# Kernel tuning notes

Hardware: AMD Instinct MI355X
Metric: run time of the kernel (lower is better)

Reference implementation:

```python
import jax, jax.numpy as jnp
import numpy as np

MASK_INFTY_APPROX = 1e30
B, L, D = 2, 2048, 1024
H = 16
HD = D // H  # 64
NCODE = 512


def setup_inputs() -> dict:
    key = jax.random.key(0)
    ks = jax.random.split(key, 6)
    s = 1.0 / np.sqrt(D)
    x = jax.random.normal(ks[0], (B, L, D), dtype=jnp.float32)
    Wq = jax.random.normal(ks[1], (D, D), dtype=jnp.float32) * s
    Wk = jax.random.normal(ks[2], (D, D), dtype=jnp.float32) * s
    Wv = jax.random.normal(ks[3], (D, D), dtype=jnp.float32) * s
    Wo = jax.random.normal(ks[4], (D, D), dtype=jnp.float32) * s
    codebook = jax.random.normal(ks[5], (H, NCODE, HD), dtype=jnp.float32)
    return {"x": x, "Wq": Wq, "Wk": Wk, "Wv": Wv, "Wo": Wo, "codebook": codebook}


def _vq(k, codebook):
    # k: [B,H,L,hd], codebook: [H,C,hd]
    dot = jnp.einsum('bhld,hcd->bhlc', k, codebook)
    k2 = jnp.sum(k * k, axis=-1, keepdims=True)            # [B,H,L,1]
    c2 = jnp.sum(codebook * codebook, axis=-1)             # [H,C]
    d2 = k2 - 2.0 * dot + c2[None, :, None, :]             # [B,H,L,C]
    shortcodes = jnp.argmin(d2, axis=-1)                   # [B,H,L]
    h_idx = jnp.arange(H)[None, :, None]
    c_sel = codebook[h_idx, shortcodes]                    # [B,H,L,hd]
    # straight-through quantization
    k_hat = k + jax.lax.stop_gradient(c_sel - k)
    l_commit = jnp.mean(jnp.sum((k - jax.lax.stop_gradient(c_sel)) ** 2, axis=-1))
    l_codebook = jnp.mean(jnp.sum((jax.lax.stop_gradient(k) - c_sel) ** 2, axis=-1))
    return k_hat, shortcodes, l_commit, l_codebook


def reference(x, Wq, Wk, Wv, Wo, codebook):
    q = jnp.einsum('bld,de->ble', x, Wq.T).reshape(B, L, H, HD).transpose(0, 2, 1, 3)
    k = jnp.einsum('bld,de->ble', x, Wk.T).reshape(B, L, H, HD).transpose(0, 2, 1, 3)
    v = jnp.einsum('bld,de->ble', x, Wv.T).reshape(B, L, H, HD).transpose(0, 2, 1, 3)
    k_hat, shortcodes, l_commit, l_codebook = _vq(k, codebook)
    scale = HD ** (-0.5)
    logits = jnp.einsum('bhld,bhtd->bhlt', q, k_hat) * scale  # [B,H,L,L]
    causal_mask = jnp.tril(jnp.ones((L, L), dtype=bool))
    logits = jnp.where(causal_mask[None, None], logits, -MASK_INFTY_APPROX)
    w = jax.nn.softmax(logits, axis=-1)
    attn = jnp.einsum('bhlt,bhtd->bhld', w, v)
    attn = attn.transpose(0, 2, 1, 3).reshape(B, L, D)
    out = jnp.einsum('bld,de->ble', attn, Wo.T)
    return out, l_commit, l_codebook, shortcodes
```

## Files before the change

kernel.cpp:

```cpp
#include <hip/hip_runtime.h>
#include <stdint.h>

#define BB 2
#define HH 16
#define LL 2048
#define DD 1024
#define HDD 64
#define NC 512

typedef __bf16 bf16x8 __attribute__((ext_vector_type(8)));
typedef float f32x4 __attribute__((ext_vector_type(4)));
typedef unsigned short u16x8 __attribute__((ext_vector_type(8)));

__device__ __forceinline__ unsigned short f2bf(float f) {
  union { float f; unsigned u; } v; v.f = f;
  unsigned u = v.u;
  u += 0x7fffu + ((u >> 16) & 1u);
  return (unsigned short)(u >> 16);
}
__device__ __forceinline__ float bf2f(unsigned short h) {
  union { unsigned u; float f; } v; v.u = ((unsigned)h) << 16;
  return v.f;
}

__device__ __forceinline__ void load_lds16(const unsigned short* g, unsigned short* l) {
  __builtin_amdgcn_global_load_lds((const __attribute__((address_space(1))) void*)g,
                                   (__attribute__((address_space(3))) void*)l, 16, 0, 0);
}

__global__ void cast_all(const float* __restrict__ x, const float* __restrict__ wq,
                         const float* __restrict__ wk, const float* __restrict__ wv,
                         const float* __restrict__ wo, const float* __restrict__ cb,
                         unsigned short* __restrict__ xb, unsigned short* __restrict__ xl,
                         unsigned short* __restrict__ wb, unsigned short* __restrict__ wkl,
                         unsigned short* __restrict__ wob, unsigned short* __restrict__ cbb,
                         unsigned short* __restrict__ cbl, float* __restrict__ lsum) {
  long i = (long)blockIdx.x * blockDim.x + threadIdx.x;
  if (i == 0) lsum[0] = 0.f;
  const long NX = 4194304, NW = 1048576, NCB = 524288;
  const long TOT = NX + 4 * NW + NCB;
  for (long t = i; t < TOT; t += (long)gridDim.x * blockDim.x) {
    if (t < NX) {
      float v = x[t];
      unsigned short hi = f2bf(v);
      xb[t] = hi;
      xl[t] = f2bf(v - bf2f(hi));
    } else if (t < NX + NW) {
      wb[t - NX] = f2bf(wq[t - NX]);
    } else if (t < NX + 2 * NW) {
      long idx = t - NX - NW;
      float v = wk[idx];
      unsigned short hi = f2bf(v);
      wb[NW + idx] = hi;
      wkl[idx] = f2bf(v - bf2f(hi));
    } else if (t < NX + 3 * NW) {
      wb[t - NX] = f2bf(wv[t - NX - 2 * NW]);
    } else if (t < NX + 4 * NW) {
      wob[t - NX - 3 * NW] = f2bf(wo[t - NX - 3 * NW]);
    } else {
      long idx = t - NX - 4 * NW;
      float v = cb[idx];
      unsigned short hi = f2bf(v);
      cbb[idx] = hi;
      cbl[idx] = f2bf(v - bf2f(hi));
    }
  }
}

__global__ void c2_kernel(const float* __restrict__ cb, float* __restrict__ c2) {
  int i = blockIdx.x * blockDim.x + threadIdx.x;
  if (i >= HH * NC) return;
  const float* r = cb + (long)i * HDD;
  double s = 0.0;
  for (int j = 0; j < HDD; j++) s += (double)r[j] * (double)r[j];
  c2[i] = (float)s;
}

__global__ __launch_bounds__(256) void gemm_qv(
    const unsigned short* __restrict__ xb, const unsigned short* __restrict__ wb,
    unsigned short* __restrict__ qb, unsigned short* __restrict__ vt) {
  __shared__ __align__(16) unsigned short As[128 * 32];
  __shared__ __align__(16) unsigned short Bs[128 * 32];
  int tid = threadIdx.x;
  int wave = tid >> 6, lane = tid & 63;
  int quad = lane >> 4, col = lane & 15;
  int m0 = blockIdx.y * 128;
  int n0 = blockIdx.x * 128 + (blockIdx.x >= 8 ? 1024 : 0);
  f32x4 acc[4][4] = {};
  int row_in = (wave << 4) + (lane >> 2);
  int seg = lane & 3;
  const unsigned short* gA0 = xb + (long)(m0 + row_in) * DD + seg * 8;
  const unsigned short* gA1 = xb + (long)(m0 + 64 + row_in) * DD + seg * 8;
  const unsigned short* gB0 = wb + (long)(n0 + row_in) * DD + seg * 8;
  const unsigned short* gB1 = wb + (long)(n0 + 64 + row_in) * DD + seg * 8;
  unsigned short* lA0 = As + wave * 512;
  unsigned short* lA1 = As + 2048 + wave * 512;
  unsigned short* lB0 = Bs + wave * 512;
  unsigned short* lB1 = Bs + 2048 + wave * 512;
  int wm = wave & 1, wn = wave >> 1;
  const unsigned short* pa = As + (wm * 64 + col) * 32 + quad * 8;
  const unsigned short* pb = Bs + (wn * 64 + col) * 32 + quad * 8;
  for (int kk = 0; kk < DD; kk += 32) {
    __syncthreads();
    load_lds16(gA0 + kk, lA0);
    load_lds16(gA1 + kk, lA1);
    load_lds16(gB0 + kk, lB0);
    load_lds16(gB1 + kk, lB1);
    __syncthreads();
    bf16x8 af[4], bfr[4];
    for (int t = 0; t < 4; t++) af[t]  = *(const bf16x8*)(pa + t * 512);
    for (int t = 0; t < 4; t++) bfr[t] = *(const bf16x8*)(pb + t * 512);
    for (int mt = 0; mt < 4; mt++)
      for (int nt = 0; nt < 4; nt++)
        acc[mt][nt] = __builtin_amdgcn_mfma_f32_16x16x32_bf16(af[mt], bfr[nt], acc[mt][nt], 0, 0, 0);
  }
  for (int mt = 0; mt < 4; mt++)
    for (int nt = 0; nt < 4; nt++) {
      int mbase = m0 + wm * 64 + mt * 16 + quad * 4;
      int n = n0 + wn * 64 + nt * 16 + col;
      int which = n >> 10, e = n & 1023;
      int h = e >> 6, hd = e & 63;
      for (int r = 0; r < 4; r++) {
        int m = mbase + r;
        int b = m >> 11, l = m & 2047;
        unsigned short val = f2bf(acc[mt][nt][r]);
        long bh = (long)(b * HH + h);
        if (which == 0)      qb[(bh * LL + l) * HDD + hd] = val;
        else                 vt[(bh * HDD + hd) * LL + l] = val;
      }
    }
}

__global__ __launch_bounds__(256) void kgemm_split(
    const unsigned short* __restrict__ xb, const unsigned short* __restrict__ xl,
    const unsigned short* __restrict__ wb, const unsigned short* __restrict__ wkl,
    float* __restrict__ kf) {
  __shared__ __align__(16) unsigned short Ah[128 * 32];
  __shared__ __align__(16) unsigned short Al[128 * 32];
  __shared__ __align__(16) unsigned short Bh[64 * 32];
  __shared__ __align__(16) unsigned short Bl[64 * 32];
  int tid = threadIdx.x;
  int wave = tid >> 6, lane = tid & 63;
  int quad = lane >> 4, col = lane & 15;
  int n0 = blockIdx.x * 64;
  int m0 = blockIdx.y * 128;
  f32x4 acc[4][2] = {};
  int row_in = (wave << 4) + (lane >> 2);
  int seg = lane & 3;
  const unsigned short* gAh0 = xb + (long)(m0 + row_in) * DD + seg * 8;
  const unsigned short* gAh1 = xb + (long)(m0 + 64 + row_in) * DD + seg * 8;
  const unsigned short* gAl0 = xl + (long)(m0 + row_in) * DD + seg * 8;
  const unsigned short* gAl1 = xl + (long)(m0 + 64 + row_in) * DD + seg * 8;
  const unsigned short* gBh  = wb + (long)(1048576 + (long)(n0 + row_in) * DD) + seg * 8;
  const unsigned short* gBl  = wkl + (long)(n0 + row_in) * DD + seg * 8;
  unsigned short* lAh0 = Ah + wave * 512;
  unsigned short* lAh1 = Ah + 2048 + wave * 512;
  unsigned short* lAl0 = Al + wave * 512;
  unsigned short* lAl1 = Al + 2048 + wave * 512;
  unsigned short* lBh  = Bh + wave * 512;
  unsigned short* lBl  = Bl + wave * 512;
  int wm = wave & 1, wn = wave >> 1;
  const unsigned short* pah = Ah + (wm * 64 + col) * 32 + quad * 8;
  const unsigned short* pal = Al + (wm * 64 + col) * 32 + quad * 8;
  const unsigned short* pbh = Bh + (wn * 32 + col) * 32 + quad * 8;
  const unsigned short* pbl = Bl + (wn * 32 + col) * 32 + quad * 8;
  for (int kk = 0; kk < DD; kk += 32) {
    __syncthreads();
    load_lds16(gAh0 + kk, lAh0);
    load_lds16(gAh1 + kk, lAh1);
    load_lds16(gAl0 + kk, lAl0);
    load_lds16(gAl1 + kk, lAl1);
    load_lds16(gBh + kk, lBh);
    load_lds16(gBl + kk, lBl);
    __syncthreads();
    bf16x8 ah[4], al[4], bhf[2], blf[2];
    for (int t = 0; t < 4; t++) ah[t] = *(const bf16x8*)(pah + t * 512);
    for (int t = 0; t < 4; t++) al[t] = *(const bf16x8*)(pal + t * 512);
    for (int t = 0; t < 2; t++) bhf[t] = *(const bf16x8*)(pbh + t * 512);
    for (int t = 0; t < 2; t++) blf[t] = *(const bf16x8*)(pbl + t * 512);
    for (int mt = 0; mt < 4; mt++)
      for (int nt = 0; nt < 2; nt++) {
        acc[mt][nt] = __builtin_amdgcn_mfma_f32_16x16x32_bf16(ah[mt], bhf[nt], acc[mt][nt], 0, 0, 0);
        acc[mt][nt] = __builtin_amdgcn_mfma_f32_16x16x32_bf16(ah[mt], blf[nt], acc[mt][nt], 0, 0, 0);
        acc[mt][nt] = __builtin_amdgcn_mfma_f32_16x16x32_bf16(al[mt], bhf[nt], acc[mt][nt], 0, 0, 0);
      }
  }
  int h = blockIdx.x;
  for (int mt = 0; mt < 4; mt++)
    for (int nt = 0; nt < 2; nt++) {
      int mbase = m0 + wm * 64 + mt * 16 + quad * 4;
      int hd = wn * 32 + nt * 16 + col;
      for (int r = 0; r < 4; r++) {
        int m = mbase + r;
        int b = m >> 11, l = m & 2047;
        kf[((long)(b * HH + h) * LL + l) * HDD + hd] = acc[mt][nt][r];
      }
    }
}

__global__ __launch_bounds__(256) void vq_mfma(
    const float* __restrict__ kf, const float* __restrict__ cb,
    const float* __restrict__ c2, const unsigned short* __restrict__ cbb,
    const unsigned short* __restrict__ cbl,
    unsigned short* __restrict__ khat, float* __restrict__ scodes,
    float* __restrict__ lsum) {
  __shared__ __align__(16) unsigned short CbH[2][32 * 72];
  __shared__ __align__(16) unsigned short CbL[2][32 * 72];
  __shared__ __align__(16) float Cs[NC];
  __shared__ int finalIdx[128];
  int tid = threadIdx.x, wave = tid >> 6, lane = tid & 63;
  int quad = lane >> 4, col = lane & 15;
  int rb = blockIdx.x;
  int bh = blockIdx.y;
  int h = bh & 15;
  int rbase = rb * 128 + wave * 32;
  const float* c2h = c2 + h * NC;
  Cs[tid] = c2h[tid];
  Cs[tid + 256] = c2h[tid + 256];

  bf16x8 bhf[2][2], blf[2][2];
  float k2g[2];
#pragma unroll
  for (int g = 0; g < 2; g++) {
    const float* kp = kf + ((long)bh * LL + rbase + g * 16 + col) * HDD + quad * 8;
    float4 t0 = *(const float4*)(kp);
    float4 t1 = *(const float4*)(kp + 4);
    float4 t2 = *(const float4*)(kp + 32);
    float4 t3 = *(const float4*)(kp + 36);
    float fv[16];
    fv[0]=t0.x; fv[1]=t0.y; fv[2]=t0.z; fv[3]=t0.w;
    fv[4]=t1.x; fv[5]=t1.y; fv[6]=t1.z; fv[7]=t1.w;
    fv[8]=t2.x; fv[9]=t2.y; fv[10]=t2.z; fv[11]=t2.w;
    fv[12]=t3.x; fv[13]=t3.y; fv[14]=t3.z; fv[15]=t3.w;
    float k2 = 0.f;
#pragma unroll
    for (int j = 0; j < 16; j++) k2 = fmaf(fv[j], fv[j], k2);
    k2 += __shfl_xor(k2, 16);
    k2 += __shfl_xor(k2, 32);
    k2g[g] = k2;
    u16x8 h0, h1, l0, l1;
#pragma unroll
    for (int j = 0; j < 8; j++) {
      unsigned short hi = f2bf(fv[j]);
      h0[j] = hi; l0[j] = f2bf(fv[j] - bf2f(hi));
      unsigned short hi2 = f2bf(fv[8 + j]);
      h1[j] = hi2; l1[j] = f2bf(fv[8 + j] - bf2f(hi2));
    }
    bhf[g][0] = __builtin_bit_cast(bf16x8, h0);
    bhf[g][1] = __builtin_bit_cast(bf16x8, h1);
    blf[g][0] = __builtin_bit_cast(bf16x8, l0);
    blf[g][1] = __builtin_bit_cast(bf16x8, l1);
  }
  const unsigned short* cbbh = cbb + (long)h * NC * HDD;
  const unsigned short* cblh = cbl + (long)h * NC * HDD;

  int srow = tid >> 3;
  int sseg = (tid & 7) * 8;
  const unsigned short* gH = cbbh + (long)srow * HDD + sseg;
  const unsigned short* gL = cblh + (long)srow * HDD + sseg;
  int ldsOff = srow * 72 + sseg;

  {
    u16x8 ph = *(const u16x8*)(gH);
    u16x8 pl = *(const u16x8*)(gL);
    *(u16x8*)(CbH[0] + ldsOff) = ph;
    *(u16x8*)(CbL[0] + ldsOff) = pl;
  }
  __syncthreads();

  float b1v[2] = {1e38f, 1e38f}, b2v[2] = {1e38f, 1e38f};
  int b1i[2] = {0x7fffffff, 0x7fffffff}, b2i[2] = {0x7fffffff, 0x7fffffff};
  for (int t = 0; t < 16; t++) {
    int cur = t & 1;
    u16x8 nh, nl;
    if (t < 15) {
      nh = *(const u16x8*)(gH + (t + 1) * 32 * HDD);
      nl = *(const u16x8*)(gL + (t + 1) * 32 * HDD);
    }
#pragma unroll
    for (int s = 0; s < 2; s++) {
      const unsigned short* rp = CbH[cur] + (s * 16 + col) * 72 + quad * 8;
      const unsigned short* rq = CbL[cur] + (s * 16 + col) * 72 + quad * 8;
      bf16x8 ah0 = *(const bf16x8*)(rp);
      bf16x8 ah1 = *(const bf16x8*)(rp + 32);
      bf16x8 al0 = *(const bf16x8*)(rq);
      bf16x8 al1 = *(const bf16x8*)(rq + 32);
      f32x4 aP0 = {}, aQ0 = {}, aP1 = {}, aQ1 = {};
      aP0 = __builtin_amdgcn_mfma_f32_16x16x32_bf16(ah0, bhf[0][0], aP0, 0, 0, 0);
      aQ0 = __builtin_amdgcn_mfma_f32_16x16x32_bf16(ah1, bhf[0][1], aQ0, 0, 0, 0);
      aP1 = __builtin_amdgcn_mfma_f32_16x16x32_bf16(ah0, bhf[1][0], aP1, 0, 0, 0);
      aQ1 = __builtin_amdgcn_mfma_f32_16x16x32_bf16(ah1, bhf[1][1], aQ1, 0, 0, 0);
      aP0 = __builtin_amdgcn_mfma_f32_16x16x32_bf16(al0, bhf[0][0], aP0, 0, 0, 0);
      aQ0 = __builtin_amdgcn_mfma_f32_16x16x32_bf16(al1, bhf[0][1], aQ0, 0, 0, 0);
      aP1 = __builtin_amdgcn_mfma_f32_16x16x32_bf16(al0, bhf[1][0], aP1, 0, 0, 0);
      aQ1 = __builtin_amdgcn_mfma_f32_16x16x32_bf16(al1, bhf[1][1], aQ1, 0, 0, 0);
      aP0 = __builtin_amdgcn_mfma_f32_16x16x32_bf16(ah0, blf[0][0], aP0, 0, 0, 0);
      aQ0 = __builtin_amdgcn_mfma_f32_16x16x32_bf16(ah1, blf[0][1], aQ0, 0, 0, 0);
      aP1 = __builtin_amdgcn_mfma_f32_16x16x32_bf16(ah0, blf[1][0], aP1, 0, 0, 0);
      aQ1 = __builtin_amdgcn_mfma_f32_16x16x32_bf16(ah1, blf[1][1], aQ1, 0, 0, 0);
      f32x4 c2v = *(const f32x4*)(Cs + t * 32 + s * 16 + quad * 4);
#pragma unroll
      for (int r = 0; r < 4; r++) {
        int idx = t * 32 + s * 16 + quad * 4 + r;
        float v0 = c2v[r] - 2.0f * (aP0[r] + aQ0[r]);
        if (v0 < b1v[0]) { b2v[0] = b1v[0]; b2i[0] = b1i[0]; b1v[0] = v0; b1i[0] = idx; }
        else if (v0 < b2v[0]) { b2v[0] = v0; b2i[0] = idx; }
        float v1 = c2v[r] - 2.0f * (aP1[r] + aQ1[r]);
        if (v1 < b1v[1]) { b2v[1] = b1v[1]; b2i[1] = b1i[1]; b1v[1] = v1; b1i[1] = idx; }
        else if (v1 < b2v[1]) { b2v[1] = v1; b2i[1] = idx; }
      }
    }
    if (t < 15) {
      *(u16x8*)(CbH[cur ^ 1] + ldsOff) = nh;
      *(u16x8*)(CbL[cur ^ 1] + ldsOff) = nl;
    }
    __syncthreads();
  }
  const float DMARG = 0.015625f;
  float partT = 0.f;
#pragma unroll
  for (int g = 0; g < 2; g++) {
    float v1 = b1v[g], v2 = b2v[g];
    int i1 = b1i[g], i2 = b2i[g];
#pragma unroll
    for (int d = 16; d <= 32; d <<= 1) {
      float o1v = __shfl_xor(v1, d); int o1i = __shfl_xor(i1, d);
      float o2v = __shfl_xor(v2, d); int o2i = __shfl_xor(i2, d);
      if (o1v < v1 || (o1v == v1 && o1i < i1)) {
        float nv; int ni;
        if (v1 < o2v || (v1 == o2v && i1 < o2i)) { nv = v1; ni = i1; }
        else { nv = o2v; ni = o2i; }
        v1 = o1v; i1 = o1i; v2 = nv; i2 = ni;
      } else {
        if (o1v < v2 || (o1v == v2 && o1i < i2)) { v2 = o1v; i2 = o1i; }
      }
    }
    bool trig = (v2 - v1 <= DMARG);
    float part;
    int widx = i1;
    if (__any(trig)) {
      const float* kpr = kf + ((long)bh * LL + rbase + g * 16 + col) * HDD + quad * 8;
      float4 f0 = *(const float4*)(kpr);
      float4 f1 = *(const float4*)(kpr + 4);
      float4 f2 = *(const float4*)(kpr + 32);
      float4 f3 = *(const float4*)(kpr + 36);
      const float* c1p = cb + ((long)h * NC + i1) * HDD + quad * 8;
      const float* c2p = cb + ((long)h * NC + i2) * HDD + quad * 8;
      float4 a0 = *(const float4*)(c1p);
      float4 a1 = *(const float4*)(c1p + 4);
      float4 a2 = *(const float4*)(c1p + 32);
      float4 a3 = *(const float4*)(c1p + 36);
      float4 e0 = *(const float4*)(c2p);
      float4 e1 = *(const float4*)(c2p + 4);
      float4 e2 = *(const float4*)(c2p + 32);
      float4 e3 = *(const float4*)(c2p + 36);
      float s1 = 0.f, s2 = 0.f;
#pragma unroll
      for (int j = 0; j < 4; j++) {
        float d;
        d = ((const float*)&f0)[j] - ((const float*)&a0)[j]; s1 = fmaf(d, d, s1);
        d = ((const float*)&f1)[j] - ((const float*)&a1)[j]; s1 = fmaf(d, d, s1);
        d = ((const float*)&f2)[j] - ((const float*)&a2)[j]; s1 = fmaf(d, d, s1);
        d = ((const float*)&f3)[j] - ((const float*)&a3)[j]; s1 = fmaf(d, d, s1);
        d = ((const float*)&f0)[j] - ((const float*)&e0)[j]; s2 = fmaf(d, d, s2);
        d = ((const float*)&f1)[j] - ((const float*)&e1)[j]; s2 = fmaf(d, d, s2);
        d = ((const float*)&f2)[j] - ((const float*)&e2)[j]; s2 = fmaf(d, d, s2);
        d = ((const float*)&f3)[j] - ((const float*)&e3)[j]; s2 = fmaf(d, d, s2);
      }
      s1 += __shfl_xor(s1, 16); s1 += __shfl_xor(s1, 32);
      s2 += __shfl_xor(s2, 16); s2 += __shfl_xor(s2, 32);
      if (trig) {
        if (s2 < s1 || (s2 == s1 && i2 < i1)) { widx = i2; part = s2; }
        else { widx = i1; part = s1; }
      } else {
        part = k2g[g] + v1;
      }
    } else {
      part = k2g[g] + v1;
    }
    if (quad == 0) partT += part;
    if (lane < 16) {
      int row_local = wave * 32 + g * 16 + lane;
      scodes[(long)bh * LL + rb * 128 + row_local] = (float)widx;
      finalIdx[row_local] = widx;
    }
  }
  partT += __shfl_xor(partT, 1);  partT += __shfl_xor(partT, 2);
  partT += __shfl_xor(partT, 4);  partT += __shfl_xor(partT, 8);
  partT += __shfl_xor(partT, 16); partT += __shfl_xor(partT, 32);
  if (lane == 0) atomicAdd(lsum, partT);
  __syncthreads();
  {
    int r = tid >> 1, p = (tid & 1) * 32;
    int code = finalIdx[r];
    const unsigned short* src = cbb + ((long)h * NC + code) * HDD + p;
    unsigned short* dst = khat + ((long)bh * LL + rb * 128 + r) * HDD + p;
    *(u16x8*)(dst)      = *(const u16x8*)(src);
    *(u16x8*)(dst + 8)  = *(const u16x8*)(src + 8);
    *(u16x8*)(dst + 16) = *(const u16x8*)(src + 16);
    *(u16x8*)(dst + 24) = *(const u16x8*)(src + 24);
  }
}

__global__ __launch_bounds__(256) void attn_kernel(
    const unsigned short* __restrict__ qb, const unsigned short* __restrict__ khat,
    const unsigned short* __restrict__ vt, unsigned short* __restrict__ attnb) {
  __shared__ __align__(16) unsigned short Pbuf[4][2][16 * 72];
  __shared__ __align__(16) unsigned short Kbuf[64 * 72];
  __shared__ __align__(16) unsigned short Vbuf[64 * 72];
  int tid = threadIdx.x, wave = tid >> 6, lane = tid & 63;
  int quad = lane >> 4, col = lane & 15;
  int pi = blockIdx.x;
  int bh = blockIdx.y;
  int b = bh >> 4, h = bh & 15;
  int ta = pi, tb = 31 - pi;
  int qbA = ta * 64 + wave * 16;
  int qbB = tb * 64 + wave * 16;
  const unsigned short* qrA = qb + ((long)bh * LL + qbA + col) * HDD;
  const unsigned short* qrB = qb + ((long)bh * LL + qbB + col) * HDD;
  bf16x8 aqA0 = *(const bf16x8*)(qrA + quad * 8);
  bf16x8 aqA1 = *(const bf16x8*)(qrA + 32 + quad * 8);
  bf16x8 aqB0 = *(const bf16x8*)(qrB + quad * 8);
  bf16x8 aqB1 = *(const bf16x8*)(qrB + 32 + quad * 8);
  float lA[4] = {0.f, 0.f, 0.f, 0.f}, lB[4] = {0.f, 0.f, 0.f, 0.f};
  f32x4 oA[4] = {}, oB[4] = {};
  unsigned short* PA = Pbuf[wave][0];
  unsigned short* PB = Pbuf[wave][1];
  const unsigned short* kh = khat + (long)bh * LL * HDD;
  const unsigned short* vh = vt + (long)bh * HDD * LL;
  int srow = tid >> 2, sc = (tid & 3) * 8;
  const unsigned short* gK = kh + (long)srow * HDD + sc;
  const unsigned short* gV = vh + (long)srow * LL + sc;
  unsigned short* lK = Kbuf + srow * 72 + sc;
  unsigned short* lV = Vbuf + srow * 72 + sc;
  const float SCL = 0.18033688011112042f;
  for (int kt = 0; kt <= tb; kt++) {
    int kbase = kt * 64;
    bool actA = (kt <= ta);
    __syncthreads();
    {
      const unsigned short* srcK = gK + (long)kbase * HDD;
      const unsigned short* srcV = gV + kbase;
      *(u16x8*)lK        = *(const u16x8*)(srcK);
      *(u16x8*)(lK + 32) = *(const u16x8*)(srcK + 32);
      *(u16x8*)lV        = *(const u16x8*)(srcV);
      *(u16x8*)(lV + 32) = *(const u16x8*)(srcV + 32);
    }
    __syncthreads();
    f32x4 zA[4], zB[4];
    for (int nt = 0; nt < 4; nt++) {
      const unsigned short* krow = Kbuf + (nt * 16 + col) * 72;
      bf16x8 k0 = *(const bf16x8*)(krow + quad * 8);
      bf16x8 k1 = *(const bf16x8*)(krow + 32 + quad * 8);
      f32x4 z = {};
      z = __builtin_amdgcn_mfma_f32_16x16x32_bf16(aqB0, k0, z, 0, 0, 0);
      z = __builtin_amdgcn_mfma_f32_16x16x32_bf16(aqB1, k1, z, 0, 0, 0);
      zB[nt] = z;
      if (actA) {
        f32x4 y = {};
        y = __builtin_amdgcn_mfma_f32_16x16x32_bf16(aqA0, k0, y, 0, 0, 0);
        y = __builtin_amdgcn_mfma_f32_16x16x32_bf16(aqA1, k1, y, 0, 0, 0);
        zA[nt] = y;
      }
    }
    for (int nt = 0; nt < 4; nt++) {
      int key = kbase + nt * 16 + col;
      for (int r = 0; r < 4; r++) {
        float sc2 = zB[nt][r] * SCL;
        if (kt == tb && key > qbB + quad * 4 + r) sc2 = -1e30f;
        float p = exp2f(sc2);
        lB[r] += p;
        PB[(quad * 4 + r) * 72 + nt * 16 + col] = __builtin_bit_cast(unsigned short, (__bf16)p);
      }
    }
    if (actA) {
      for (int nt = 0; nt < 4; nt++) {
        int key = kbase + nt * 16 + col;
        for (int r = 0; r < 4; r++) {
          float sc2 = zA[nt][r] * SCL;
          if (kt == ta && key > qbA + quad * 4 + r) sc2 = -1e30f;
          float p = exp2f(sc2);
          lA[r] += p;
          PA[(quad * 4 + r) * 72 + nt * 16 + col] = __builtin_bit_cast(unsigned short, (__bf16)p);
        }
      }
    }
    bf16x8 apB0 = *(const bf16x8*)(PB + col * 72 + quad * 8);
    bf16x8 apB1 = *(const bf16x8*)(PB + col * 72 + 32 + quad * 8);
    bf16x8 apA0, apA1;
    if (actA) {
      apA0 = *(const bf16x8*)(PA + col * 72 + quad * 8);
      apA1 = *(const bf16x8*)(PA + col * 72 + 32 + quad * 8);
    }
    for (int nt = 0; nt < 4; nt++) {
      const unsigned short* vrow = Vbuf + (nt * 16 + col) * 72;
      bf16x8 v0 = *(const bf16x8*)(vrow + quad * 8);
      bf16x8 v1 = *(const bf16x8*)(vrow + 32 + quad * 8);
      oB[nt] = __builtin_amdgcn_mfma_f32_16x16x32_bf16(apB0, v0, oB[nt], 0, 0, 0);
      oB[nt] = __builtin_amdgcn_mfma_f32_16x16x32_bf16(apB1, v1, oB[nt], 0, 0, 0);
      if (actA) {
        oA[nt] = __builtin_amdgcn_mfma_f32_16x16x32_bf16(apA0, v0, oA[nt], 0, 0, 0);
        oA[nt] = __builtin_amdgcn_mfma_f32_16x16x32_bf16(apA1, v1, oA[nt], 0, 0, 0);
      }
    }
  }
  float invA[4], invB[4];
  for (int r = 0; r < 4; r++) {
    float t = lA[r];
    t += __shfl_xor(t, 1); t += __shfl_xor(t, 2);
    t += __shfl_xor(t, 4); t += __shfl_xor(t, 8);
    invA[r] = 1.0f / t;
    float u = lB[r];
    u += __shfl_xor(u, 1); u += __shfl_xor(u, 2);
    u += __shfl_xor(u, 4); u += __shfl_xor(u, 8);
    invB[r] = 1.0f / u;
  }
  for (int r = 0; r < 4; r++) {
    int rowA = qbA + quad * 4 + r;
    int rowB = qbB + quad * 4 + r;
    for (int nt = 0; nt < 4; nt++) {
      int hd = nt * 16 + col;
      attnb[((long)b * LL + rowA) * DD + h * HDD + hd] = f2bf(oA[nt][r] * invA[r]);
      attnb[((long)b * LL + rowB) * DD + h * HDD + hd] = f2bf(oB[nt][r] * invB[r]);
    }
  }
}

__global__ __launch_bounds__(256) void gemm_out(
    const unsigned short* __restrict__ attnb, const unsigned short* __restrict__ wob,
    float* __restrict__ out) {
  __shared__ __align__(16) unsigned short As[128 * 32];
  __shared__ __align__(16) unsigned short Bs[128 * 32];
  int tid = threadIdx.x;
  int wave = tid >> 6, lane = tid & 63;
  int quad = lane >> 4, col = lane & 15;
  int m0 = blockIdx.y * 128;
  int n0 = blockIdx.x * 128;
  f32x4 acc[4][4] = {};
  int row_in = (wave << 4) + (lane >> 2);
  int seg = lane & 3;
  const unsigned short* gA0 = attnb + (long)(m0 + row_in) * DD + seg * 8;
  const unsigned short* gA1 = attnb + (long)(m0 + 64 + row_in) * DD + seg * 8;
  const unsigned short* gB0 = wob + (long)(n0 + row_in) * DD + seg * 8;
  const unsigned short* gB1 = wob + (long)(n0 + 64 + row_in) * DD + seg * 8;
  unsigned short* lA0 = As + wave * 512;
  unsigned short* lA1 = As + 2048 + wave * 512;
  unsigned short* lB0 = Bs + wave * 512;
  unsigned short* lB1 = Bs + 2048 + wave * 512;
  int wm = wave & 1, wn = wave >> 1;
  const unsigned short* pa = As + (wm * 64 + col) * 32 + quad * 8;
  const unsigned short* pb = Bs + (wn * 64 + col) * 32 + quad * 8;
  for (int kk = 0; kk < DD; kk += 32) {
    __syncthreads();
    load_lds16(gA0 + kk, lA0);
    load_lds16(gA1 + kk, lA1);
    load_lds16(gB0 + kk, lB0);
    load_lds16(gB1 + kk, lB1);
    __syncthreads();
    bf16x8 af[4], bfr[4];
    for (int t = 0; t < 4; t++) af[t]  = *(const bf16x8*)(pa + t * 512);
    for (int t = 0; t < 4; t++) bfr[t] = *(const bf16x8*)(pb + t * 512);
    for (int mt = 0; mt < 4; mt++)
      for (int nt = 0; nt < 4; nt++)
        acc[mt][nt] = __builtin_amdgcn_mfma_f32_16x16x32_bf16(af[mt], bfr[nt], acc[mt][nt], 0, 0, 0);
  }
  for (int mt = 0; mt < 4; mt++)
    for (int nt = 0; nt < 4; nt++) {
      int mbase = m0 + wm * 64 + mt * 16 + quad * 4;
      int n = n0 + wn * 64 + nt * 16 + col;
      for (int r = 0; r < 4; r++)
        out[(long)(mbase + r) * DD + n] = acc[mt][nt][r];
    }
}

__global__ void finalize(const float* __restrict__ lsum, float* __restrict__ out) {
  if (threadIdx.x == 0) {
    float v = lsum[0] / (float)(BB * HH * LL);
    out[4194304] = v;
    out[4194305] = v;
  }
}

extern "C" void kernel_launch(void* const* d_in, const int* in_sizes, int n_in,
                              void* d_out, int out_size, void* d_ws, size_t ws_size,
                              hipStream_t stream) {
  const float* x  = (const float*)d_in[0];
  const float* wq = (const float*)d_in[1];
  const float* wk = (const float*)d_in[2];
  const float* wv = (const float*)d_in[3];
  const float* wo = (const float*)d_in[4];
  const float* cb = (const float*)d_in[5];
  float* out = (float*)d_out;

  char* ws = (char*)d_ws;
  size_t off = 0;
  auto alloc = [&](size_t bytes) {
    void* p = ws + off;
    off = (off + bytes + 255) & ~(size_t)255;
    return p;
  };
  unsigned short* xb    = (unsigned short*)alloc(4194304 * 2);
  unsigned short* xl    = (unsigned short*)alloc(4194304 * 2);
  unsigned short* wb    = (unsigned short*)alloc(3145728 * 2);
  unsigned short* wkl   = (unsigned short*)alloc(1048576 * 2);
  unsigned short* wob   = (unsigned short*)alloc(1048576 * 2);
  unsigned short* cbb   = (unsigned short*)alloc(524288 * 2);
  unsigned short* cbl   = (unsigned short*)alloc(524288 * 2);
  unsigned short* qb    = (unsigned short*)alloc(4194304 * 2);
  unsigned short* vt    = (unsigned short*)alloc(4194304 * 2);
  unsigned short* khat  = (unsigned short*)alloc(4194304 * 2);
  unsigned short* attnb = (unsigned short*)alloc(4194304 * 2);
  float* kf   = (float*)alloc(4194304 * 4);
  float* c2   = (float*)alloc(8192 * 4);
  float* lsum = (float*)alloc(256);

  cast_all<<<dim3(4096), dim3(256), 0, stream>>>(x, wq, wk, wv, wo, cb, xb, xl, wb, wkl, wob, cbb, cbl, lsum);
  c2_kernel<<<dim3(32), dim3(256), 0, stream>>>(cb, c2);
  gemm_qv<<<dim3(16, 32), dim3(256), 0, stream>>>(xb, wb, qb, vt);
  kgemm_split<<<dim3(16, 32), dim3(256), 0, stream>>>(xb, xl, wb, wkl, kf);
  vq_mfma<<<dim3(16, 32), dim3(256), 0, stream>>>(kf, cb, c2, cbb, cbl, khat, out + 4194306, lsum);
  attn_kernel<<<dim3(16, 32), dim3(256), 0, stream>>>(qb, khat, vt, attnb);
  gemm_out<<<dim3(8, 32), dim3(256), 0, stream>>>(attnb, wob, out);
  finalize<<<dim3(1), dim3(64), 0, stream>>>(lsum, out);
}
```

Before: 314.4 us.

## Split paired causal attention tiles into one tile per block with XCD-aware mapping

The attention kernel used to pair query tiles pi and 31-pi inside one block to balance causal work. It now launches one block per query tile (1024 blocks), remapped so that blocks sharing a (batch, head) land on the same XCD for L2 reuse of K/V. It also prefetches the next K/V tile into registers while computing the current one. This reduces register pressure and raises occupancy, but gives up the built-in load balance and relies on the hardware scheduler to absorb the uneven per-block work.

```diff
diff --git a/kernel.cpp b/kernel.cpp
--- a/kernel.cpp
+++ b/kernel.cpp
@@ -405,27 +405,23 @@
 __global__ __launch_bounds__(256) void attn_kernel(
     const unsigned short* __restrict__ qb, const unsigned short* __restrict__ khat,
     const unsigned short* __restrict__ vt, unsigned short* __restrict__ attnb) {
-  __shared__ __align__(16) unsigned short Pbuf[4][2][16 * 72];
   __shared__ __align__(16) unsigned short Kbuf[64 * 72];
   __shared__ __align__(16) unsigned short Vbuf[64 * 72];
+  __shared__ __align__(16) unsigned short Pbuf[4][16 * 72];
   int tid = threadIdx.x, wave = tid >> 6, lane = tid & 63;
   int quad = lane >> 4, col = lane & 15;
-  int pi = blockIdx.x;
-  int bh = blockIdx.y;
+  int id = blockIdx.y * 32 + blockIdx.x;
+  int xcd = id & 7, idx = id >> 3;
+  int bh = xcd * 4 + (idx >> 5);
+  int qt = idx & 31;
   int b = bh >> 4, h = bh & 15;
-  int ta = pi, tb = 31 - pi;
-  int qbA = ta * 64 + wave * 16;
-  int qbB = tb * 64 + wave * 16;
-  const unsigned short* qrA = qb + ((long)bh * LL + qbA + col) * HDD;
-  const unsigned short* qrB = qb + ((long)bh * LL + qbB + col) * HDD;
-  bf16x8 aqA0 = *(const bf16x8*)(qrA + quad * 8);
-  bf16x8 aqA1 = *(const bf16x8*)(qrA + 32 + quad * 8);
-  bf16x8 aqB0 = *(const bf16x8*)(qrB + quad * 8);
-  bf16x8 aqB1 = *(const bf16x8*)(qrB + 32 + quad * 8);
-  float lA[4] = {0.f, 0.f, 0.f, 0.f}, lB[4] = {0.f, 0.f, 0.f, 0.f};
-  f32x4 oA[4] = {}, oB[4] = {};
-  unsigned short* PA = Pbuf[wave][0];
-  unsigned short* PB = Pbuf[wave][1];
+  int qbase = qt * 64 + wave * 16;
+  const unsigned short* qr = qb + ((long)bh * LL + qbase + col) * HDD;
+  bf16x8 aq0 = *(const bf16x8*)(qr + quad * 8);
+  bf16x8 aq1 = *(const bf16x8*)(qr + 32 + quad * 8);
+  float l[4] = {0.f, 0.f, 0.f, 0.f};
+  f32x4 o[4] = {};
+  unsigned short* P = Pbuf[wave];
   const unsigned short* kh = khat + (long)bh * LL * HDD;
   const unsigned short* vh = vt + (long)bh * HDD * LL;
   int srow = tid >> 2, sc = (tid & 3) * 8;
@@ -434,94 +430,68 @@
   unsigned short* lK = Kbuf + srow * 72 + sc;
   unsigned short* lV = Vbuf + srow * 72 + sc;
   const float SCL = 0.18033688011112042f;
-  for (int kt = 0; kt <= tb; kt++) {
+  u16x8 rk0 = *(const u16x8*)(gK);
+  u16x8 rk1 = *(const u16x8*)(gK + 32);
+  u16x8 rv0 = *(const u16x8*)(gV);
+  u16x8 rv1 = *(const u16x8*)(gV + 32);
+  for (int kt = 0; kt <= qt; kt++) {
+    __syncthreads();
+    *(u16x8*)lK        = rk0;
+    *(u16x8*)(lK + 32) = rk1;
+    *(u16x8*)lV        = rv0;
+    *(u16x8*)(lV + 32) = rv1;
+    __syncthreads();
+    if (kt < qt) {
+      const unsigned short* nK = gK + (long)(kt + 1) * 64 * HDD;
+      const unsigned short* nV = gV + (kt + 1) * 64;
+      rk0 = *(const u16x8*)(nK);
+      rk1 = *(const u16x8*)(nK + 32);
+      rv0 = *(const u16x8*)(nV);
+      rv1 = *(const u16x8*)(nV + 32);
+    }
     int kbase = kt * 64;
-    bool actA = (kt <= ta);
-    __syncthreads();
-    {
-      const unsigned short* srcK = gK + (long)kbase * HDD;
-      const unsigned short* srcV = gV + kbase;
-      *(u16x8*)lK        = *(const u16x8*)(srcK);
-      *(u16x8*)(lK + 32) = *(const u16x8*)(srcK + 32);
-      *(u16x8*)lV        = *(const u16x8*)(srcV);
-      *(u16x8*)(lV + 32) = *(const u16x8*)(srcV + 32);
-    }
-    __syncthreads();
-    f32x4 zA[4], zB[4];
+    f32x4 z[4];
     for (int nt = 0; nt < 4; nt++) {
       const unsigned short* krow = Kbuf + (nt * 16 + col) * 72;
       bf16x8 k0 = *(const bf16x8*)(krow + quad * 8);
       bf16x8 k1 = *(const bf16x8*)(krow + 32 + quad * 8);
-      f32x4 z = {};
-      z = __builtin_amdgcn_mfma_f32_16x16x32_bf16(aqB0, k0, z, 0, 0, 0);
-      z = __builtin_amdgcn_mfma_f32_16x16x32_bf16(aqB1, k1, z, 0, 0, 0);
-      zB[nt] = z;
-      if (actA) {
-        f32x4 y = {};
-        y = __builtin_amdgcn_mfma_f32_16x16x32_bf16(aqA0, k0, y, 0, 0, 0);
-        y = __builtin_amdgcn_mfma_f32_16x16x32_bf16(aqA1, k1, y, 0, 0, 0);
-        zA[nt] = y;
-      }
+      f32x4 zz = {};
+      zz = __builtin_amdgcn_mfma_f32_16x16x32_bf16(aq0, k0, zz, 0, 0, 0);
+      zz = __builtin_amdgcn_mfma_f32_16x16x32_bf16(aq1, k1, zz, 0, 0, 0);
+      z[nt] = zz;
     }
     for (int nt = 0; nt < 4; nt++) {
       int key = kbase + nt * 16 + col;
       for (int r = 0; r < 4; r++) {
-        float sc2 = zB[nt][r] * SCL;
-        if (kt == tb && key > qbB + quad * 4 + r) sc2 = -1e30f;
+        float sc2 = z[nt][r] * SCL;
+        if (kt == qt && key > qbase + quad * 4 + r) sc2 = -1e30f;
         float p = exp2f(sc2);
-        lB[r] += p;
-        PB[(quad * 4 + r) * 72 + nt * 16 + col] = __builtin_bit_cast(unsigned short, (__bf16)p);
-      }
-    }
-    if (actA) {
-      for (int nt = 0; nt < 4; nt++) {
-        int key = kbase + nt * 16 + col;
-        for (int r = 0; r < 4; r++) {
-          float sc2 = zA[nt][r] * SCL;
-          if (kt == ta && key > qbA + quad * 4 + r) sc2 = -1e30f;
-          float p = exp2f(sc2);
-          lA[r] += p;
-          PA[(quad * 4 + r) * 72 + nt * 16 + col] = __builtin_bit_cast(unsigned short, (__bf16)p);
-        }
-      }
-    }
-    bf16x8 apB0 = *(const bf16x8*)(PB + col * 72 + quad * 8);
-    bf16x8 apB1 = *(const bf16x8*)(PB + col * 72 + 32 + quad * 8);
-    bf16x8 apA0, apA1;
-    if (actA) {
-      apA0 = *(const bf16x8*)(PA + col * 72 + quad * 8);
-      apA1 = *(const bf16x8*)(PA + col * 72 + 32 + quad * 8);
-    }
+        l[r] += p;
+        P[(quad * 4 + r) * 72 + nt * 16 + col] = __builtin_bit_cast(unsigned short, (__bf16)p);
+      }
+    }
+    bf16x8 ap0 = *(const bf16x8*)(P + col * 72 + quad * 8);
+    bf16x8 ap1 = *(const bf16x8*)(P + col * 72 + 32 + quad * 8);
     for (int nt = 0; nt < 4; nt++) {
       const unsigned short* vrow = Vbuf + (nt * 16 + col) * 72;
       bf16x8 v0 = *(const bf16x8*)(vrow + quad * 8);
       bf16x8 v1 = *(const bf16x8*)(vrow + 32 + quad * 8);
-      oB[nt] = __builtin_amdgcn_mfma_f32_16x16x32_bf16(apB0, v0, oB[nt], 0, 0, 0);
-      oB[nt] = __builtin_amdgcn_mfma_f32_16x16x32_bf16(apB1, v1, oB[nt], 0, 0, 0);
-      if (actA) {
-        oA[nt] = __builtin_amdgcn_mfma_f32_16x16x32_bf16(apA0, v0, oA[nt], 0, 0, 0);
-        oA[nt] = __builtin_amdgcn_mfma_f32_16x16x32_bf16(apA1, v1, oA[nt], 0, 0, 0);
-      }
-    }
-  }
-  float invA[4], invB[4];
+      o[nt] = __builtin_amdgcn_mfma_f32_16x16x32_bf16(ap0, v0, o[nt], 0, 0, 0);
+      o[nt] = __builtin_amdgcn_mfma_f32_16x16x32_bf16(ap1, v1, o[nt], 0, 0, 0);
+    }
+  }
+  float inv[4];
   for (int r = 0; r < 4; r++) {
-    float t = lA[r];
+    float t = l[r];
     t += __shfl_xor(t, 1); t += __shfl_xor(t, 2);
     t += __shfl_xor(t, 4); t += __shfl_xor(t, 8);
-    invA[r] = 1.0f / t;
-    float u = lB[r];
-    u += __shfl_xor(u, 1); u += __shfl_xor(u, 2);
-    u += __shfl_xor(u, 4); u += __shfl_xor(u, 8);
-    invB[r] = 1.0f / u;
+    inv[r] = 1.0f / t;
   }
   for (int r = 0; r < 4; r++) {
-    int rowA = qbA + quad * 4 + r;
-    int rowB = qbB + quad * 4 + r;
+    int row = qbase + quad * 4 + r;
     for (int nt = 0; nt < 4; nt++) {
       int hd = nt * 16 + col;
-      attnb[((long)b * LL + rowA) * DD + h * HDD + hd] = f2bf(oA[nt][r] * invA[r]);
-      attnb[((long)b * LL + rowB) * DD + h * HDD + hd] = f2bf(oB[nt][r] * invB[r]);
+      attnb[((long)b * LL + row) * DD + h * HDD + hd] = f2bf(o[nt][r] * inv[r]);
     }
   }
 }
@@ -619,7 +589,7 @@
   gemm_qv<<<dim3(16, 32), dim3(256), 0, stream>>>(xb, wb, qb, vt);
   kgemm_split<<<dim3(16, 32), dim3(256), 0, stream>>>(xb, xl, wb, wkl, kf);
   vq_mfma<<<dim3(16, 32), dim3(256), 0, stream>>>(kf, cb, c2, cbb, cbl, khat, out + 4194306, lsum);
-  attn_kernel<<<dim3(16, 32), dim3(256), 0, stream>>>(qb, khat, vt, attnb);
+  attn_kernel<<<dim3(32, 32), dim3(256), 0, stream>>>(qb, khat, vt, attnb);
   gemm_out<<<dim3(8, 32), dim3(256), 0, stream>>>(attnb, wob, out);
   finalize<<<dim3(1), dim3(64), 0, stream>>>(lsum, out);
 }
```

Measured after the change: 324.4 us. 1.03x slower.

## Fuse K projection GEMM with VQ, remap blocks per XCD, prefetch attention tiles

Applied to the files above, without the earlier changes.

Merges the split-precision K GEMM and the VQ codebook search into one kernel. The fp32 K tile is kept in shared memory instead of being written to and re-read from a global kf buffer, which also removes one launch. Block indices in both the fused kernel and attention are remapped so blocks sharing a head/batch land on the same XCD for better L2 locality. Attention now register-prefetches the next K/V tile to overlap global loads with compute. The cost is much larger LDS use (about 55 KB per block), which may lower occupancy.

```diff
diff --git a/kernel.cpp b/kernel.cpp
--- a/kernel.cpp
+++ b/kernel.cpp
@@ -131,19 +131,40 @@
     }
 }
 
-__global__ __launch_bounds__(256) void kgemm_split(
+__global__ __launch_bounds__(256) void kvq(
     const unsigned short* __restrict__ xb, const unsigned short* __restrict__ xl,
     const unsigned short* __restrict__ wb, const unsigned short* __restrict__ wkl,
-    float* __restrict__ kf) {
-  __shared__ __align__(16) unsigned short Ah[128 * 32];
-  __shared__ __align__(16) unsigned short Al[128 * 32];
-  __shared__ __align__(16) unsigned short Bh[64 * 32];
-  __shared__ __align__(16) unsigned short Bl[64 * 32];
+    const float* __restrict__ cb, const float* __restrict__ c2,
+    const unsigned short* __restrict__ cbb, const unsigned short* __restrict__ cbl,
+    unsigned short* __restrict__ khat, float* __restrict__ scodes,
+    float* __restrict__ lsum) {
+  __shared__ __align__(16) char smem[55808];
+  unsigned short* Ah = (unsigned short*)smem;
+  unsigned short* Al = (unsigned short*)(smem + 8192);
+  unsigned short* Bh = (unsigned short*)(smem + 16384);
+  unsigned short* Bl = (unsigned short*)(smem + 20480);
+  float* kfL = (float*)smem;
+  unsigned short* CbHb = (unsigned short*)(smem + 34816);
+  unsigned short* CbLb = (unsigned short*)(smem + 44032);
+  float* Cs = (float*)(smem + 53248);
+  int* finalIdx = (int*)(smem + 55296);
+
   int tid = threadIdx.x;
   int wave = tid >> 6, lane = tid & 63;
   int quad = lane >> 4, col = lane & 15;
-  int n0 = blockIdx.x * 64;
-  int m0 = blockIdx.y * 128;
+  int id = blockIdx.y * 16 + blockIdx.x;
+  int xcd = id & 7, sidx = id >> 3;
+  int mt4 = xcd * 4 + (sidx >> 4);
+  int h = sidx & 15;
+  int m0 = mt4 * 128;
+  int n0 = h * 64;
+  int bgl = m0 >> 11;
+  int l0 = m0 & 2047;
+  long bh = (long)(bgl * HH + h);
+
+  Cs[tid] = c2[h * NC + tid];
+  Cs[tid + 256] = c2[h * NC + 256 + tid];
+
   f32x4 acc[4][2] = {};
   int row_in = (wave << 4) + (lane >> 2);
   int seg = lane & 3;
@@ -185,44 +206,32 @@
         acc[mt][nt] = __builtin_amdgcn_mfma_f32_16x16x32_bf16(al[mt], bhf[nt], acc[mt][nt], 0, 0, 0);
       }
   }
-  int h = blockIdx.x;
+  __syncthreads();
+  const unsigned short* cbbh = cbb + (long)h * NC * HDD;
+  const unsigned short* cblh = cbl + (long)h * NC * HDD;
+  int srow = tid >> 3;
+  int sseg = (tid & 7) * 8;
+  const unsigned short* gH = cbbh + (long)srow * HDD + sseg;
+  const unsigned short* gL = cblh + (long)srow * HDD + sseg;
+  int ldsOff = srow * 72 + sseg;
+  u16x8 ph0 = *(const u16x8*)(gH);
+  u16x8 pl0 = *(const u16x8*)(gL);
   for (int mt = 0; mt < 4; mt++)
     for (int nt = 0; nt < 2; nt++) {
-      int mbase = m0 + wm * 64 + mt * 16 + quad * 4;
+      int rbasew = wm * 64 + mt * 16 + quad * 4;
       int hd = wn * 32 + nt * 16 + col;
-      for (int r = 0; r < 4; r++) {
-        int m = mbase + r;
-        int b = m >> 11, l = m & 2047;
-        kf[((long)(b * HH + h) * LL + l) * HDD + hd] = acc[mt][nt][r];
-      }
-    }
-}
-
-__global__ __launch_bounds__(256) void vq_mfma(
-    const float* __restrict__ kf, const float* __restrict__ cb,
-    const float* __restrict__ c2, const unsigned short* __restrict__ cbb,
-    const unsigned short* __restrict__ cbl,
-    unsigned short* __restrict__ khat, float* __restrict__ scodes,
-    float* __restrict__ lsum) {
-  __shared__ __align__(16) unsigned short CbH[2][32 * 72];
-  __shared__ __align__(16) unsigned short CbL[2][32 * 72];
-  __shared__ __align__(16) float Cs[NC];
-  __shared__ int finalIdx[128];
-  int tid = threadIdx.x, wave = tid >> 6, lane = tid & 63;
-  int quad = lane >> 4, col = lane & 15;
-  int rb = blockIdx.x;
-  int bh = blockIdx.y;
-  int h = bh & 15;
-  int rbase = rb * 128 + wave * 32;
-  const float* c2h = c2 + h * NC;
-  Cs[tid] = c2h[tid];
-  Cs[tid + 256] = c2h[tid + 256];
-
-  bf16x8 bhf[2][2], blf[2][2];
+      for (int r = 0; r < 4; r++)
+        kfL[(rbasew + r) * 68 + hd] = acc[mt][nt][r];
+    }
+  *(u16x8*)(CbHb + ldsOff) = ph0;
+  *(u16x8*)(CbLb + ldsOff) = pl0;
+  __syncthreads();
+
+  bf16x8 bfh[2][2], bfl[2][2];
   float k2g[2];
 #pragma unroll
   for (int g = 0; g < 2; g++) {
-    const float* kp = kf + ((long)bh * LL + rbase + g * 16 + col) * HDD + quad * 8;
+    const float* kp = kfL + (wave * 32 + g * 16 + col) * 68 + quad * 8;
     float4 t0 = *(const float4*)(kp);
     float4 t1 = *(const float4*)(kp + 4);
     float4 t2 = *(const float4*)(kp + 32);
@@ -238,36 +247,19 @@
     k2 += __shfl_xor(k2, 16);
     k2 += __shfl_xor(k2, 32);
     k2g[g] = k2;
-    u16x8 h0, h1, l0, l1;
+    u16x8 h0, h1, l0u, l1u;
 #pragma unroll
     for (int j = 0; j < 8; j++) {
       unsigned short hi = f2bf(fv[j]);
-      h0[j] = hi; l0[j] = f2bf(fv[j] - bf2f(hi));
+      h0[j] = hi; l0u[j] = f2bf(fv[j] - bf2f(hi));
       unsigned short hi2 = f2bf(fv[8 + j]);
-      h1[j] = hi2; l1[j] = f2bf(fv[8 + j] - bf2f(hi2));
-    }
-    bhf[g][0] = __builtin_bit_cast(bf16x8, h0);
-    bhf[g][1] = __builtin_bit_cast(bf16x8, h1);
-    blf[g][0] = __builtin_bit_cast(bf16x8, l0);
-    blf[g][1] = __builtin_bit_cast(bf16x8, l1);
-  }
-  const unsigned short* cbbh = cbb + (long)h * NC * HDD;
-  const unsigned short* cblh = cbl + (long)h * NC * HDD;
-
-  int srow = tid >> 3;
-  int sseg = (tid & 7) * 8;
-  const unsigned short* gH = cbbh + (long)srow * HDD + sseg;
-  const unsigned short* gL = cblh + (long)srow * HDD + sseg;
-  int ldsOff = srow * 72 + sseg;
-
-  {
-    u16x8 ph = *(const u16x8*)(gH);
-    u16x8 pl = *(const u16x8*)(gL);
-    *(u16x8*)(CbH[0] + ldsOff) = ph;
-    *(u16x8*)(CbL[0] + ldsOff) = pl;
-  }
-  __syncthreads();
-
+      h1[j] = hi2; l1u[j] = f2bf(fv[8 + j] - bf2f(hi2));
+    }
+    bfh[g][0] = __builtin_bit_cast(bf16x8, h0);
+    bfh[g][1] = __builtin_bit_cast(bf16x8, h1);
+    bfl[g][0] = __builtin_bit_cast(bf16x8, l0u);
+    bfl[g][1] = __builtin_bit_cast(bf16x8, l1u);
+  }
   float b1v[2] = {1e38f, 1e38f}, b2v[2] = {1e38f, 1e38f};
   int b1i[2] = {0x7fffffff, 0x7fffffff}, b2i[2] = {0x7fffffff, 0x7fffffff};
   for (int t = 0; t < 16; t++) {
@@ -277,27 +269,29 @@
       nh = *(const u16x8*)(gH + (t + 1) * 32 * HDD);
       nl = *(const u16x8*)(gL + (t + 1) * 32 * HDD);
     }
+    const unsigned short* CbHc = CbHb + cur * 2304;
+    const unsigned short* CbLc = CbLb + cur * 2304;
 #pragma unroll
     for (int s = 0; s < 2; s++) {
-      const unsigned short* rp = CbH[cur] + (s * 16 + col) * 72 + quad * 8;
-      const unsigned short* rq = CbL[cur] + (s * 16 + col) * 72 + quad * 8;
+      const unsigned short* rp = CbHc + (s * 16 + col) * 72 + quad * 8;
+      const unsigned short* rq = CbLc + (s * 16 + col) * 72 + quad * 8;
       bf16x8 ah0 = *(const bf16x8*)(rp);
       bf16x8 ah1 = *(const bf16x8*)(rp + 32);
       bf16x8 al0 = *(const bf16x8*)(rq);
       bf16x8 al1 = *(const bf16x8*)(rq + 32);
       f32x4 aP0 = {}, aQ0 = {}, aP1 = {}, aQ1 = {};
-      aP0 = __builtin_amdgcn_mfma_f32_16x16x32_bf16(ah0, bhf[0][0], aP0, 0, 0, 0);
-      aQ0 = __builtin_amdgcn_mfma_f32_16x16x32_bf16(ah1, bhf[0][1], aQ0, 0, 0, 0);
-      aP1 = __builtin_amdgcn_mfma_f32_16x16x32_bf16(ah0, bhf[1][0], aP1, 0, 0, 0);
-      aQ1 = __builtin_amdgcn_mfma_f32_16x16x32_bf16(ah1, bhf[1][1], aQ1, 0, 0, 0);
-      aP0 = __builtin_amdgcn_mfma_f32_16x16x32_bf16(al0, bhf[0][0], aP0, 0, 0, 0);
-      aQ0 = __builtin_amdgcn_mfma_f32_16x16x32_bf16(al1, bhf[0][1], aQ0, 0, 0, 0);
-      aP1 = __builtin_amdgcn_mfma_f32_16x16x32_bf16(al0, bhf[1][0], aP1, 0, 0, 0);
-      aQ1 = __builtin_amdgcn_mfma_f32_16x16x32_bf16(al1, bhf[1][1], aQ1, 0, 0, 0);
-      aP0 = __builtin_amdgcn_mfma_f32_16x16x32_bf16(ah0, blf[0][0], aP0, 0, 0, 0);
-      aQ0 = __builtin_amdgcn_mfma_f32_16x16x32_bf16(ah1, blf[0][1], aQ0, 0, 0, 0);
-      aP1 = __builtin_amdgcn_mfma_f32_16x16x32_bf16(ah0, blf[1][0], aP1, 0, 0, 0);
-      aQ1 = __builtin_amdgcn_mfma_f32_16x16x32_bf16(ah1, blf[1][1], aQ1, 0, 0, 0);
+      aP0 = __builtin_amdgcn_mfma_f32_16x16x32_bf16(ah0, bfh[0][0], aP0, 0, 0, 0);
+      aQ0 = __builtin_amdgcn_mfma_f32_16x16x32_bf16(ah1, bfh[0][1], aQ0, 0, 0, 0);
+      aP1 = __builtin_amdgcn_mfma_f32_16x16x32_bf16(ah0, bfh[1][0], aP1, 0, 0, 0);
+      aQ1 = __builtin_amdgcn_mfma_f32_16x16x32_bf16(ah1, bfh[1][1], aQ1, 0, 0, 0);
+      aP0 = __builtin_amdgcn_mfma_f32_16x16x32_bf16(al0, bfh[0][0], aP0, 0, 0, 0);
+      aQ0 = __builtin_amdgcn_mfma_f32_16x16x32_bf16(al1, bfh[0][1], aQ0, 0, 0, 0);
+      aP1 = __builtin_amdgcn_mfma_f32_16x16x32_bf16(al0, bfh[1][0], aP1, 0, 0, 0);
+      aQ1 = __builtin_amdgcn_mfma_f32_16x16x32_bf16(al1, bfh[1][1], aQ1, 0, 0, 0);
+      aP0 = __builtin_amdgcn_mfma_f32_16x16x32_bf16(ah0, bfl[0][0], aP0, 0, 0, 0);
+      aQ0 = __builtin_amdgcn_mfma_f32_16x16x32_bf16(ah1, bfl[0][1], aQ0, 0, 0, 0);
+      aP1 = __builtin_amdgcn_mfma_f32_16x16x32_bf16(ah0, bfl[1][0], aP1, 0, 0, 0);
+      aQ1 = __builtin_amdgcn_mfma_f32_16x16x32_bf16(ah1, bfl[1][1], aQ1, 0, 0, 0);
       f32x4 c2v = *(const f32x4*)(Cs + t * 32 + s * 16 + quad * 4);
 #pragma unroll
       for (int r = 0; r < 4; r++) {
@@ -311,8 +305,8 @@
       }
     }
     if (t < 15) {
-      *(u16x8*)(CbH[cur ^ 1] + ldsOff) = nh;
-      *(u16x8*)(CbL[cur ^ 1] + ldsOff) = nl;
+      *(u16x8*)(CbHb + (cur ^ 1) * 2304 + ldsOff) = nh;
+      *(u16x8*)(CbLb + (cur ^ 1) * 2304 + ldsOff) = nl;
     }
     __syncthreads();
   }
@@ -339,7 +333,7 @@
     float part;
     int widx = i1;
     if (__any(trig)) {
-      const float* kpr = kf + ((long)bh * LL + rbase + g * 16 + col) * HDD + quad * 8;
+      const float* kpr = kfL + (wave * 32 + g * 16 + col) * 68 + quad * 8;
       float4 f0 = *(const float4*)(kpr);
       float4 f1 = *(const float4*)(kpr + 4);
       float4 f2 = *(const float4*)(kpr + 32);
@@ -381,7 +375,7 @@
     if (quad == 0) partT += part;
     if (lane < 16) {
       int row_local = wave * 32 + g * 16 + lane;
-      scodes[(long)bh * LL + rb * 128 + row_local] = (float)widx;
+      scodes[bh * LL + l0 + row_local] = (float)widx;
       finalIdx[row_local] = widx;
     }
   }
@@ -394,7 +388,7 @@
     int r = tid >> 1, p = (tid & 1) * 32;
     int code = finalIdx[r];
     const unsigned short* src = cbb + ((long)h * NC + code) * HDD + p;
-    unsigned short* dst = khat + ((long)bh * LL + rb * 128 + r) * HDD + p;
+    unsigned short* dst = khat + (bh * LL + l0 + r) * HDD + p;
     *(u16x8*)(dst)      = *(const u16x8*)(src);
     *(u16x8*)(dst + 8)  = *(const u16x8*)(src + 8);
     *(u16x8*)(dst + 16) = *(const u16x8*)(src + 16);
@@ -410,8 +404,10 @@
   __shared__ __align__(16) unsigned short Vbuf[64 * 72];
   int tid = threadIdx.x, wave = tid >> 6, lane = tid & 63;
   int quad = lane >> 4, col = lane & 15;
-  int pi = blockIdx.x;
-  int bh = blockIdx.y;
+  int id = blockIdx.y * 16 + blockIdx.x;
+  int xcd = id & 7, sidx = id >> 3;
+  int bh = xcd * 4 + (sidx >> 4);
+  int pi = sidx & 15;
   int b = bh >> 4, h = bh & 15;
   int ta = pi, tb = 31 - pi;
   int qbA = ta * 64 + wave * 16;
@@ -434,19 +430,27 @@
   unsigned short* lK = Kbuf + srow * 72 + sc;
   unsigned short* lV = Vbuf + srow * 72 + sc;
   const float SCL = 0.18033688011112042f;
+  u16x8 rk0 = *(const u16x8*)(gK);
+  u16x8 rk1 = *(const u16x8*)(gK + 32);
+  u16x8 rv0 = *(const u16x8*)(gV);
+  u16x8 rv1 = *(const u16x8*)(gV + 32);
   for (int kt = 0; kt <= tb; kt++) {
     int kbase = kt * 64;
     bool actA = (kt <= ta);
     __syncthreads();
-    {
-      const unsigned short* srcK = gK + (long)kbase * HDD;
-      const unsigned short* srcV = gV + kbase;
-      *(u16x8*)lK        = *(const u16x8*)(srcK);
-      *(u16x8*)(lK + 32) = *(const u16x8*)(srcK + 32);
-      *(u16x8*)lV        = *(const u16x8*)(srcV);
-      *(u16x8*)(lV + 32) = *(const u16x8*)(srcV + 32);
-    }
-    __syncthreads();
+    *(u16x8*)lK        = rk0;
+    *(u16x8*)(lK + 32) = rk1;
+    *(u16x8*)lV        = rv0;
+    *(u16x8*)(lV + 32) = rv1;
+    __syncthreads();
+    if (kt < tb) {
+      const unsigned short* nK = gK + (long)(kt + 1) * 64 * HDD;
+      const unsigned short* nV = gV + (kt + 1) * 64;
+      rk0 = *(const u16x8*)(nK);
+      rk1 = *(const u16x8*)(nK + 32);
+      rv0 = *(const u16x8*)(nV);
+      rv1 = *(const u16x8*)(nV + 32);
+    }
     f32x4 zA[4], zB[4];
     for (int nt = 0; nt < 4; nt++) {
       const unsigned short* krow = Kbuf + (nt * 16 + col) * 72;
@@ -610,15 +614,13 @@
   unsigned short* vt    = (unsigned short*)alloc(4194304 * 2);
   unsigned short* khat  = (unsigned short*)alloc(4194304 * 2);
   unsigned short* attnb = (unsigned short*)alloc(4194304 * 2);
-  float* kf   = (float*)alloc(4194304 * 4);
   float* c2   = (float*)alloc(8192 * 4);
   float* lsum = (float*)alloc(256);
 
   cast_all<<<dim3(4096), dim3(256), 0, stream>>>(x, wq, wk, wv, wo, cb, xb, xl, wb, wkl, wob, cbb, cbl, lsum);
   c2_kernel<<<dim3(32), dim3(256), 0, stream>>>(cb, c2);
   gemm_qv<<<dim3(16, 32), dim3(256), 0, stream>>>(xb, wb, qb, vt);
-  kgemm_split<<<dim3(16, 32), dim3(256), 0, stream>>>(xb, xl, wb, wkl, kf);
-  vq_mfma<<<dim3(16, 32), dim3(256), 0, stream>>>(kf, cb, c2, cbb, cbl, khat, out + 4194306, lsum);
+  kvq<<<dim3(16, 32), dim3(256), 0, stream>>>(xb, xl, wb, wkl, cb, c2, cbb, cbl, khat, out + 4194306, lsum);
   attn_kernel<<<dim3(16, 32), dim3(256), 0, stream>>>(qb, khat, vt, attnb);
   gemm_out<<<dim3(8, 32), dim3(256), 0, stream>>>(attnb, wob, out);
   finalize<<<dim3(1), dim3(64), 0, stream>>>(lsum, out);
```

Result: faster. 300.3 us (-4.5%).
